# Optimization experiments

Hardware: AMD Instinct MI355X
Metric: run time of the kernel (lower is better)

Reference implementation:

```python
import jax, jax.numpy as jnp
import numpy as np
from jax import lax

ALPHA = 2.0
T_TAGS = 8  # number of distinct connects tags
ANCHOR_POS_FACTOR = jnp.array([1.0, 1.0], dtype=jnp.float32)
POS_FACTOR = [2.0, 1.0]  # [4,4,4,2,1][-2:]
NEG_FACTOR = [2.0, 1.0]


def setup_inputs() -> dict:
    key = jax.random.key(0)
    ks = jax.random.split(key, 10)
    B, A, M = 2, 2, 64
    Da, Db = 128, 64
    logits_a = jax.random.normal(ks[0], (B, A, Da, Da, Da), dtype=jnp.float32)
    logits_b = jax.random.normal(ks[1], (B, A, Db, Db, Db), dtype=jnp.float32)
    # GT prob maps: background labeled -1 (negmask), sparse positives labeled 1
    prob_a = jnp.where(jax.random.uniform(ks[2], (B, A, Da, Da, Da)) < 0.995, -1.0, 1.0).astype(jnp.float32)
    prob_b = jnp.where(jax.random.uniform(ks[3], (B, A, Db, Db, Db)) < 0.995, -1.0, 1.0).astype(jnp.float32)
    connects_a = jax.random.randint(ks[4], (B, A, Da, Da, Da), 0, T_TAGS, dtype=jnp.int32)
    connects_b = jax.random.randint(ks[5], (B, A, Db, Db, Db), 0, T_TAGS, dtype=jnp.int32)
    def make_coord(k, D):
        ka, kz = jax.random.split(k)
        anc = jax.random.randint(ka, (B, M, 1), 0, A, dtype=jnp.int32)
        sp = jax.random.randint(kz, (B, M, 3), 0, D, dtype=jnp.int32)
        c = jnp.concatenate([anc, sp], axis=-1)
        # pad last quarter of rows with -1 (invalid), as in the original padded coord lists
        c = c.at[:, 3 * M // 4:, :].set(-1)
        return c
    coord_a = make_coord(ks[6], Da)
    coord_b = make_coord(ks[7], Db)
    fnames = jnp.arange(B, dtype=jnp.float32)
    return {"logits_a": logits_a, "logits_b": logits_b, "prob_a": prob_a, "prob_b": prob_b,
            "connects_a": connects_a, "connects_b": connects_b,
            "coord_a": coord_a, "coord_b": coord_b, "fnames": fnames}


def _level_loss(logits, prob_gt, connects, coord, pos_f, neg_f):
    # ---- negative branch: sigmoid/logsigmoid elementwise + NMS maxpool mask ----
    prob = jax.nn.sigmoid(logits)
    nll = -jax.nn.log_sigmoid(-logits)  # -log(1 - sigmoid(logit))
    negmask = (prob_gt == -1.0).astype(logits.dtype)
    # max_pool3d kernel 3, stride 1, pad 1 over (D,H,W); anchors are channels
    pooled = lax.reduce_window(prob, -jnp.inf, lax.max,
                               (1, 1, 3, 3, 3), (1, 1, 1, 1, 1), 'SAME')
    max_filter = lax.stop_gradient((pooled == prob).astype(logits.dtype))
    negmask = negmask * max_filter
    w_neg = lax.stop_gradient(prob) ** ALPHA * negmask
    loss_neg = jnp.sum(nll * w_neg) * neg_f
    count_neg = jnp.sum(w_neg)
    wsum_neg = jnp.sum(w_neg) * neg_f

    # ---- positive branch: batched gather at coords (pad rows = -1) ----
    B, M, _ = coord.shape
    valid = coord[:, :, 0] > -1                       # [B, M]
    c = jnp.where(valid[..., None], coord, 0)         # safe indices
    b_idx = jnp.arange(B)[:, None]
    lp = logits[b_idx, c[..., 0], c[..., 1], c[..., 2], c[..., 3]]  # [B, M]
    pp = jax.nn.sigmoid(lp)
    w1 = (1.0 - lax.stop_gradient(pp)) ** ALPHA
    w2 = ANCHOR_POS_FACTOR[c[..., 0]]
    vf = valid.astype(logits.dtype)
    loss_pos = -jnp.sum(jax.nn.log_sigmoid(lp) * w1 * w2 * vf) * pos_f
    count_pos = jnp.sum(w1 * vf)
    wsum_pos = jnp.sum(w1 * w2 * vf) * pos_f

    # ---- connects-tag segment-min grouping (torch.unique + per-tag min) ----
    tags = connects[b_idx, c[..., 0], c[..., 1], c[..., 2], c[..., 3]]  # [B, M]
    seg = (jnp.arange(B, dtype=jnp.int32)[:, None] * T_TAGS + tags).reshape(-1)
    data = jnp.where(valid, w1, jnp.inf).reshape(-1)
    seg_min = jax.ops.segment_min(data, seg, num_segments=B * T_TAGS).reshape(B, T_TAGS)
    seg_min = jnp.where(jnp.isfinite(seg_min), seg_min, -1.0)  # absent tags -> -1 sentinel
    return loss_pos, loss_neg, count_pos, count_neg, wsum_pos, wsum_neg, seg_min


def reference(logits_a, logits_b, prob_a, prob_b, connects_a, connects_b, coord_a, coord_b, fnames):
    ra = _level_loss(logits_a, prob_a, connects_a, coord_a, POS_FACTOR[0], NEG_FACTOR[0])
    rb = _level_loss(logits_b, prob_b, connects_b, coord_b, POS_FACTOR[1], NEG_FACTOR[1])
    cls_loss_pos = ra[0] + rb[0]
    cls_loss_neg = ra[1] + rb[1]
    count_pos = ra[2] + rb[2]
    count_neg = ra[3] + rb[3]
    wsum_pos = ra[4] + rb[4]
    wsum_neg = ra[5] + rb[5]
    # pred_prob summary: per (level, sample, tag) min positive weight; fnames broadcast alongside
    pred_prob_min = jnp.stack([ra[6], rb[6]], axis=0)  # [2, B, T_TAGS]
    return (cls_loss_pos, cls_loss_neg, count_pos, count_neg, wsum_pos, wsum_neg, pred_prob_min)
```

## Files before the change

kernel.cpp:

```cpp
#include <hip/hip_runtime.h>
#include <math.h>


#define NBLK_A 1024
#define NBLK_B 256
#define NBLK_TOTAL (NBLK_A + NBLK_B + 1)

__device__ __forceinline__ float fmax3(float a, float b, float c) {
    return fmaxf(a, fmaxf(b, c));
}

__global__ __launch_bounds__(256, 3) void fused_kernel(
    const float* __restrict__ la, const float* __restrict__ lb,
    const float* __restrict__ ga, const float* __restrict__ gb,
    const int* __restrict__ conn_a, const int* __restrict__ conn_b,
    const int* __restrict__ coord_a, const int* __restrict__ coord_b,
    float* __restrict__ ws, float* __restrict__ out)
{
    __shared__ float tile[12800];
    __shared__ float sred[8];
    const int bid = blockIdx.x;
    const int t = threadIdx.x;
    float loss = 0.0f, wsum = 0.0f;
    int accIdx = -1;

    if (bid < NBLK_A) {
        accIdx = 0;
        const int vol = bid >> 8;
        const int ti = bid & 255;
        const int y0 = (ti & 15) << 3;
        const int z0 = (ti >> 4) << 3;
        const float* base = la + vol * (128 * 128 * 128);

        float4 stg[13];
        int us[13];
#pragma unroll
        for (int i = 0; i < 13; ++i) {
            int u = t + 256 * i; u = u < 3199 ? u : 3199;
            us[i] = u;
            int r = u >> 5, xq = u & 31;
            int rz = r / 10, ry = r - rz * 10;
            int gy = y0 - 1 + ry; gy = gy < 0 ? 0 : (gy > 127 ? 127 : gy);
            int gz = z0 - 1 + rz; gz = gz < 0 ? 0 : (gz > 127 ? 127 : gz);
            stg[i] = *(const float4*)(base + (gz * 128 + gy) * 128 + (xq << 2));
        }
#pragma unroll
        for (int i = 0; i < 13; ++i)
            *(float4*)(tile + (us[i] << 2)) = stg[i];
        __syncthreads();

        const int xq = t & 31, w = t >> 5;
        const int x0 = xq << 2;
        const int y = y0 + w;
        const float* gbase = ga + ((vol * 128 + z0) * 128 + y) * 128 + x0;
        float4 g[8];
#pragma unroll
        for (int zi = 0; zi < 8; ++zi) g[zi] = *(const float4*)(gbase + zi * 16384);

        float pm[3][4];
        float cm[2][4];
#pragma unroll
        for (int p = 0; p < 10; ++p) {
            const float* r0 = tile + (p * 10 + w) * 128 + x0;
            float4 a0 = *(const float4*)(r0);
            float4 a1 = *(const float4*)(r0 + 128);
            float4 a2 = *(const float4*)(r0 + 256);
            pm[p % 3][0] = fmax3(a0.x, a1.x, a2.x);
            pm[p % 3][1] = fmax3(a0.y, a1.y, a2.y);
            pm[p % 3][2] = fmax3(a0.z, a1.z, a2.z);
            pm[p % 3][3] = fmax3(a0.w, a1.w, a2.w);
            cm[p & 1][0] = a1.x; cm[p & 1][1] = a1.y;
            cm[p & 1][2] = a1.z; cm[p & 1][3] = a1.w;
            if (p >= 2) {
                float cz0 = fmax3(pm[0][0], pm[1][0], pm[2][0]);
                float cz1 = fmax3(pm[0][1], pm[1][1], pm[2][1]);
                float cz2 = fmax3(pm[0][2], pm[1][2], pm[2][2]);
                float cz3 = fmax3(pm[0][3], pm[1][3], pm[2][3]);
                float lco = __shfl_up(cz3, 1);  if (xq == 0)  lco = cz0;
                float rco = __shfl_down(cz0, 1); if (xq == 31) rco = cz3;
                float m0 = fmax3(lco, cz0, cz1);
                float m1 = fmax3(cz0, cz1, cz2);
                float m2 = fmax3(cz1, cz2, cz3);
                float m3 = fmax3(cz2, cz3, rco);
                const float* c = cm[(p - 1) & 1];
                float4 gv = g[p - 2];
                float ms[4] = {m0, m1, m2, m3};
                float gs[4] = {gv.x, gv.y, gv.z, gv.w};
#pragma unroll
                for (int k = 0; k < 4; ++k) {
                    if (gs[k] == -1.0f && ms[k] == c[k]) {
                        float e = __expf(c[k]);
                        float u = __builtin_amdgcn_rcpf(1.0f + e);
                        float sc = e * u;
                        float wv = sc * sc;
                        wsum += wv;
                        loss += (-__logf(u)) * wv;
                    }
                }
            }
        }
    } else if (bid < NBLK_A + NBLK_B) {
        accIdx = 2;
        const int b2 = bid - NBLK_A;
        const int vol = b2 >> 6;
        const int ti = b2 & 63;
        const int y0 = (ti & 7) << 3;
        const int z0 = (ti >> 3) << 3;
        const float* base = lb + vol * (64 * 64 * 64);

        float4 stg[7];
        int us[7];
#pragma unroll
        for (int i = 0; i < 7; ++i) {
            int u = t + 256 * i; u = u < 1599 ? u : 1599;
            us[i] = u;
            int r = u >> 4, xq = u & 15;
            int rz = r / 10, ry = r - rz * 10;
            int gy = y0 - 1 + ry; gy = gy < 0 ? 0 : (gy > 63 ? 63 : gy);
            int gz = z0 - 1 + rz; gz = gz < 0 ? 0 : (gz > 63 ? 63 : gz);
            stg[i] = *(const float4*)(base + (gz * 64 + gy) * 64 + (xq << 2));
        }
#pragma unroll
        for (int i = 0; i < 7; ++i)
            *(float4*)(tile + (us[i] << 2)) = stg[i];
        __syncthreads();

        const int xq = t & 15, grp = t >> 4;
        const int x0 = xq << 2;
        const int wy = grp & 7, zh = grp >> 3;
        const int y = y0 + wy;
        const float* gbase = gb + ((vol * 64 + z0 + 4 * zh) * 64 + y) * 64 + x0;
        float4 g[4];
#pragma unroll
        for (int j = 0; j < 4; ++j) g[j] = *(const float4*)(gbase + j * 4096);

        float pm[3][4];
        float cm[2][4];
#pragma unroll
        for (int pp = 0; pp < 6; ++pp) {
            const int rz = 4 * zh + pp;
            const float* r0 = tile + (rz * 10 + wy) * 64 + x0;
            float4 a0 = *(const float4*)(r0);
            float4 a1 = *(const float4*)(r0 + 64);
            float4 a2 = *(const float4*)(r0 + 128);
            pm[pp % 3][0] = fmax3(a0.x, a1.x, a2.x);
            pm[pp % 3][1] = fmax3(a0.y, a1.y, a2.y);
            pm[pp % 3][2] = fmax3(a0.z, a1.z, a2.z);
            pm[pp % 3][3] = fmax3(a0.w, a1.w, a2.w);
            cm[pp & 1][0] = a1.x; cm[pp & 1][1] = a1.y;
            cm[pp & 1][2] = a1.z; cm[pp & 1][3] = a1.w;
            if (pp >= 2) {
                float cz0 = fmax3(pm[0][0], pm[1][0], pm[2][0]);
                float cz1 = fmax3(pm[0][1], pm[1][1], pm[2][1]);
                float cz2 = fmax3(pm[0][2], pm[1][2], pm[2][2]);
                float cz3 = fmax3(pm[0][3], pm[1][3], pm[2][3]);
                float lco = __shfl_up(cz3, 1);  if (xq == 0)  lco = cz0;
                float rco = __shfl_down(cz0, 1); if (xq == 15) rco = cz3;
                float m0 = fmax3(lco, cz0, cz1);
                float m1 = fmax3(cz0, cz1, cz2);
                float m2 = fmax3(cz1, cz2, cz3);
                float m3 = fmax3(cz2, cz3, rco);
                const float* c = cm[(pp - 1) & 1];
                float4 gv = g[pp - 2];
                float ms[4] = {m0, m1, m2, m3};
                float gs[4] = {gv.x, gv.y, gv.z, gv.w};
#pragma unroll
                for (int k = 0; k < 4; ++k) {
                    if (gs[k] == -1.0f && ms[k] == c[k]) {
                        float e = __expf(c[k]);
                        float u = __builtin_amdgcn_rcpf(1.0f + e);
                        float sc = e * u;
                        float wv = sc * sc;
                        wsum += wv;
                        loss += (-__logf(u)) * wv;
                    }
                }
            }
        }
    } else {
        float* w1s = tile;
        float* tgf = tile + 128;
        for (int level = 0; level < 2; ++level) {
            const float* logits = level ? lb : la;
            const int* conn = level ? conn_b : conn_a;
            const int* coord = level ? coord_b : coord_a;
            const int D = level ? 64 : 128;
            float li = 0.0f, ci = 0.0f;
            if (t < 128) {
                const int* c4 = coord + t * 4;
                int a = c4[0], zz = c4[1], yy = c4[2], xx = c4[3];
                bool valid = a > -1;
                int aa = valid ? a : 0, z2 = valid ? zz : 0,
                    y2 = valid ? yy : 0, x2 = valid ? xx : 0;
                int b = t >> 6;
                int off = (((b * 2 + aa) * D + z2) * D + y2) * D + x2;
                float lp = logits[off];
                int tag = conn[off];
                float s = 1.0f / (1.0f + expf(lp));
                float w1 = s * s;
                float vf = valid ? 1.0f : 0.0f;
                float sp = fmaxf(-lp, 0.0f) + log1pf(expf(-fabsf(lp)));
                li = sp * w1 * vf;
                ci = w1 * vf;
                w1s[t] = w1;
                tgf[t] = (float)(valid ? tag : -1);
            }
            for (int o = 32; o; o >>= 1) {
                li += __shfl_down(li, o);
                ci += __shfl_down(ci, o);
            }
            if ((t & 63) == 0) { sred[t >> 6] = li; sred[4 + (t >> 6)] = ci; }
            __syncthreads();
            if (t == 0) {
                atomicAdd(ws + 4 + 2 * level, sred[0] + sred[1] + sred[2] + sred[3]);
                atomicAdd(ws + 5 + 2 * level, sred[4] + sred[5] + sred[6] + sred[7]);
            }
            if (t < 16) {
                int bb = t >> 3, tg = t & 7;
                float mn = INFINITY;
                for (int i = 0; i < 64; ++i) {
                    int j = bb * 64 + i;
                    if (tgf[j] == (float)tg) mn = fminf(mn, w1s[j]);
                }
                out[6 + level * 16 + bb * 8 + tg] = isinf(mn) ? -1.0f : mn;
            }
            __syncthreads();
        }
    }

    if (accIdx >= 0) {
        for (int o = 32; o; o >>= 1) {
            loss += __shfl_down(loss, o);
            wsum += __shfl_down(wsum, o);
        }
        if ((t & 63) == 0) { sred[t >> 6] = loss; sred[4 + (t >> 6)] = wsum; }
        __syncthreads();
        if (t == 0) {
            float L = sred[0] + sred[1] + sred[2] + sred[3];
            float W = sred[4] + sred[5] + sred[6] + sred[7];
            if (L != 0.0f || W != 0.0f) {
                atomicAdd(ws + accIdx, L);
                atomicAdd(ws + accIdx + 1, W);
            }
        }
    }

    if (t == 0) {
        __threadfence();
        unsigned int old = atomicAdd((unsigned int*)(ws + 8), 1u);
        if (old == NBLK_TOTAL - 1) {
            float s0 = atomicAdd(ws + 0, 0.0f);
            float s1 = atomicAdd(ws + 1, 0.0f);
            float s2 = atomicAdd(ws + 2, 0.0f);
            float s3 = atomicAdd(ws + 3, 0.0f);
            float s4 = atomicAdd(ws + 4, 0.0f);
            float s5 = atomicAdd(ws + 5, 0.0f);
            float s6 = atomicAdd(ws + 6, 0.0f);
            float s7 = atomicAdd(ws + 7, 0.0f);
            out[0] = s4 * 2.0f + s6;
            out[1] = s0 * 2.0f + s2;
            out[2] = s5 + s7;
            out[3] = s1 + s3;
            out[4] = s5 * 2.0f + s7;
            out[5] = s1 * 2.0f + s3;
        }
    }
}

extern "C" void kernel_launch(void* const* d_in, const int* in_sizes, int n_in,
                              void* d_out, int out_size, void* d_ws, size_t ws_size,
                              hipStream_t stream) {
    const float* logits_a = (const float*)d_in[0];
    const float* logits_b = (const float*)d_in[1];
    const float* prob_a   = (const float*)d_in[2];
    const float* prob_b   = (const float*)d_in[3];
    const int*   conn_a   = (const int*)d_in[4];
    const int*   conn_b   = (const int*)d_in[5];
    const int*   coord_a  = (const int*)d_in[6];
    const int*   coord_b  = (const int*)d_in[7];
    float* out = (float*)d_out;
    float* ws  = (float*)d_ws;

    hipMemsetAsync(ws, 0, 12 * sizeof(float), stream);
    fused_kernel<<<NBLK_TOTAL, 256, 0, stream>>>(
        logits_a, logits_b, prob_a, prob_b,
        conn_a, conn_b, coord_a, coord_b, ws, out);
}
```

Baseline: 188.2 us.

## Replace LDS halo tiling with per-thread z-slice y-marching from global memory

Drops the 50KB shared-memory halo tile and its cooperative staging and barrier. Each thread now owns one z slice and marches along y, reading the three neighbouring z rows straight from global memory and relying on L1/L2 for halo reuse. Level-B block count is halved so each block covers 16 z slices, and launch bounds rise to 4 waves per SIMD because LDS no longer limits occupancy. In exchange, global and cache traffic rises, since each logit row is fetched by several threads instead of once per block.

```diff
diff --git a/kernel.cpp b/kernel.cpp
--- a/kernel.cpp
+++ b/kernel.cpp
@@ -3,22 +3,86 @@
 
 
 #define NBLK_A 1024
-#define NBLK_B 256
+#define NBLK_B 128
 #define NBLK_TOTAL (NBLK_A + NBLK_B + 1)
 
 __device__ __forceinline__ float fmax3(float a, float b, float c) {
     return fmaxf(a, fmaxf(b, c));
 }
 
-__global__ __launch_bounds__(256, 3) void fused_kernel(
+template <int D, int LOG2D, int XQ>
+__device__ __forceinline__ void neg_march(
+    const float* __restrict__ logits, const float* __restrict__ gt,
+    int vol, int z, int y0, int xq, float& loss, float& wsum)
+{
+    const int x0 = xq << 2;
+    const float* vb = logits + (vol << (3 * LOG2D));
+    const int zm = z > 0 ? z - 1 : 0;
+    const int zp = z < D - 1 ? z + 1 : z;
+    const float* pzm = vb + (zm << (2 * LOG2D));
+    const float* pz0 = vb + (z << (2 * LOG2D));
+    const float* pzp = vb + (zp << (2 * LOG2D));
+    const float* pg = gt + (vol << (3 * LOG2D)) + (z << (2 * LOG2D));
+
+    float zw[3][4];
+    float cc[2][4];
+    float4 gg[2];
+
+#pragma unroll
+    for (int s = 0; s < 10; ++s) {
+        int yy = y0 - 1 + s;
+        yy = yy < 0 ? 0 : (yy > D - 1 ? D - 1 : yy);
+        const int ro = (yy << LOG2D) + x0;
+        float4 r0 = *(const float4*)(pzm + ro);
+        float4 r1 = *(const float4*)(pz0 + ro);
+        float4 r2 = *(const float4*)(pzp + ro);
+        if (s >= 1 && s <= 8) gg[s & 1] = *(const float4*)(pg + ro);
+        zw[s % 3][0] = fmax3(r0.x, r1.x, r2.x);
+        zw[s % 3][1] = fmax3(r0.y, r1.y, r2.y);
+        zw[s % 3][2] = fmax3(r0.z, r1.z, r2.z);
+        zw[s % 3][3] = fmax3(r0.w, r1.w, r2.w);
+        cc[s & 1][0] = r1.x; cc[s & 1][1] = r1.y;
+        cc[s & 1][2] = r1.z; cc[s & 1][3] = r1.w;
+        if (s >= 2) {
+            float cz0 = fmax3(zw[0][0], zw[1][0], zw[2][0]);
+            float cz1 = fmax3(zw[0][1], zw[1][1], zw[2][1]);
+            float cz2 = fmax3(zw[0][2], zw[1][2], zw[2][2]);
+            float cz3 = fmax3(zw[0][3], zw[1][3], zw[2][3]);
+            float lco = __shfl_up(cz3, 1);   if (xq == 0)      lco = cz0;
+            float rco = __shfl_down(cz0, 1); if (xq == XQ - 1) rco = cz3;
+            float m0 = fmax3(lco, cz0, cz1);
+            float m1 = fmax3(cz0, cz1, cz2);
+            float m2 = fmax3(cz1, cz2, cz3);
+            float m3 = fmax3(cz2, cz3, rco);
+            const float* c = cc[(s - 1) & 1];
+            float4 gq = gg[(s - 1) & 1];
+            float ms[4] = {m0, m1, m2, m3};
+            float gs[4] = {gq.x, gq.y, gq.z, gq.w};
+#pragma unroll
+            for (int k = 0; k < 4; ++k) {
+                if (gs[k] == -1.0f && ms[k] == c[k]) {
+                    float e = __expf(c[k]);
+                    float u = __builtin_amdgcn_rcpf(1.0f + e);
+                    float sc = e * u;
+                    float wv = sc * sc;
+                    wsum += wv;
+                    loss += (-__logf(u)) * wv;
+                }
+            }
+        }
+    }
+}
+
+__global__ __launch_bounds__(256, 4) void fused_kernel(
     const float* __restrict__ la, const float* __restrict__ lb,
     const float* __restrict__ ga, const float* __restrict__ gb,
     const int* __restrict__ conn_a, const int* __restrict__ conn_b,
     const int* __restrict__ coord_a, const int* __restrict__ coord_b,
     float* __restrict__ ws, float* __restrict__ out)
 {
-    __shared__ float tile[12800];
     __shared__ float sred[8];
+    __shared__ float w1s[128];
+    __shared__ float tgf[128];
     const int bid = blockIdx.x;
     const int t = threadIdx.x;
     float loss = 0.0f, wsum = 0.0f;
@@ -27,159 +91,19 @@
     if (bid < NBLK_A) {
         accIdx = 0;
         const int vol = bid >> 8;
-        const int ti = bid & 255;
-        const int y0 = (ti & 15) << 3;
-        const int z0 = (ti >> 4) << 3;
-        const float* base = la + vol * (128 * 128 * 128);
-
-        float4 stg[13];
-        int us[13];
-#pragma unroll
-        for (int i = 0; i < 13; ++i) {
-            int u = t + 256 * i; u = u < 3199 ? u : 3199;
-            us[i] = u;
-            int r = u >> 5, xq = u & 31;
-            int rz = r / 10, ry = r - rz * 10;
-            int gy = y0 - 1 + ry; gy = gy < 0 ? 0 : (gy > 127 ? 127 : gy);
-            int gz = z0 - 1 + rz; gz = gz < 0 ? 0 : (gz > 127 ? 127 : gz);
-            stg[i] = *(const float4*)(base + (gz * 128 + gy) * 128 + (xq << 2));
-        }
-#pragma unroll
-        for (int i = 0; i < 13; ++i)
-            *(float4*)(tile + (us[i] << 2)) = stg[i];
-        __syncthreads();
-
-        const int xq = t & 31, w = t >> 5;
-        const int x0 = xq << 2;
-        const int y = y0 + w;
-        const float* gbase = ga + ((vol * 128 + z0) * 128 + y) * 128 + x0;
-        float4 g[8];
-#pragma unroll
-        for (int zi = 0; zi < 8; ++zi) g[zi] = *(const float4*)(gbase + zi * 16384);
-
-        float pm[3][4];
-        float cm[2][4];
-#pragma unroll
-        for (int p = 0; p < 10; ++p) {
-            const float* r0 = tile + (p * 10 + w) * 128 + x0;
-            float4 a0 = *(const float4*)(r0);
-            float4 a1 = *(const float4*)(r0 + 128);
-            float4 a2 = *(const float4*)(r0 + 256);
-            pm[p % 3][0] = fmax3(a0.x, a1.x, a2.x);
-            pm[p % 3][1] = fmax3(a0.y, a1.y, a2.y);
-            pm[p % 3][2] = fmax3(a0.z, a1.z, a2.z);
-            pm[p % 3][3] = fmax3(a0.w, a1.w, a2.w);
-            cm[p & 1][0] = a1.x; cm[p & 1][1] = a1.y;
-            cm[p & 1][2] = a1.z; cm[p & 1][3] = a1.w;
-            if (p >= 2) {
-                float cz0 = fmax3(pm[0][0], pm[1][0], pm[2][0]);
-                float cz1 = fmax3(pm[0][1], pm[1][1], pm[2][1]);
-                float cz2 = fmax3(pm[0][2], pm[1][2], pm[2][2]);
-                float cz3 = fmax3(pm[0][3], pm[1][3], pm[2][3]);
-                float lco = __shfl_up(cz3, 1);  if (xq == 0)  lco = cz0;
-                float rco = __shfl_down(cz0, 1); if (xq == 31) rco = cz3;
-                float m0 = fmax3(lco, cz0, cz1);
-                float m1 = fmax3(cz0, cz1, cz2);
-                float m2 = fmax3(cz1, cz2, cz3);
-                float m3 = fmax3(cz2, cz3, rco);
-                const float* c = cm[(p - 1) & 1];
-                float4 gv = g[p - 2];
-                float ms[4] = {m0, m1, m2, m3};
-                float gs[4] = {gv.x, gv.y, gv.z, gv.w};
-#pragma unroll
-                for (int k = 0; k < 4; ++k) {
-                    if (gs[k] == -1.0f && ms[k] == c[k]) {
-                        float e = __expf(c[k]);
-                        float u = __builtin_amdgcn_rcpf(1.0f + e);
-                        float sc = e * u;
-                        float wv = sc * sc;
-                        wsum += wv;
-                        loss += (-__logf(u)) * wv;
-                    }
-                }
-            }
-        }
+        const int rem = bid & 255;
+        const int zb = rem >> 4, yc = rem & 15;
+        neg_march<128, 7, 32>(la, ga, vol, zb * 8 + (t >> 5), yc * 8, t & 31,
+                              loss, wsum);
     } else if (bid < NBLK_A + NBLK_B) {
         accIdx = 2;
         const int b2 = bid - NBLK_A;
-        const int vol = b2 >> 6;
-        const int ti = b2 & 63;
-        const int y0 = (ti & 7) << 3;
-        const int z0 = (ti >> 3) << 3;
-        const float* base = lb + vol * (64 * 64 * 64);
-
-        float4 stg[7];
-        int us[7];
-#pragma unroll
-        for (int i = 0; i < 7; ++i) {
-            int u = t + 256 * i; u = u < 1599 ? u : 1599;
-            us[i] = u;
-            int r = u >> 4, xq = u & 15;
-            int rz = r / 10, ry = r - rz * 10;
-            int gy = y0 - 1 + ry; gy = gy < 0 ? 0 : (gy > 63 ? 63 : gy);
-            int gz = z0 - 1 + rz; gz = gz < 0 ? 0 : (gz > 63 ? 63 : gz);
-            stg[i] = *(const float4*)(base + (gz * 64 + gy) * 64 + (xq << 2));
-        }
-#pragma unroll
-        for (int i = 0; i < 7; ++i)
-            *(float4*)(tile + (us[i] << 2)) = stg[i];
-        __syncthreads();
-
-        const int xq = t & 15, grp = t >> 4;
-        const int x0 = xq << 2;
-        const int wy = grp & 7, zh = grp >> 3;
-        const int y = y0 + wy;
-        const float* gbase = gb + ((vol * 64 + z0 + 4 * zh) * 64 + y) * 64 + x0;
-        float4 g[4];
-#pragma unroll
-        for (int j = 0; j < 4; ++j) g[j] = *(const float4*)(gbase + j * 4096);
-
-        float pm[3][4];
-        float cm[2][4];
-#pragma unroll
-        for (int pp = 0; pp < 6; ++pp) {
-            const int rz = 4 * zh + pp;
-            const float* r0 = tile + (rz * 10 + wy) * 64 + x0;
-            float4 a0 = *(const float4*)(r0);
-            float4 a1 = *(const float4*)(r0 + 64);
-            float4 a2 = *(const float4*)(r0 + 128);
-            pm[pp % 3][0] = fmax3(a0.x, a1.x, a2.x);
-            pm[pp % 3][1] = fmax3(a0.y, a1.y, a2.y);
-            pm[pp % 3][2] = fmax3(a0.z, a1.z, a2.z);
-            pm[pp % 3][3] = fmax3(a0.w, a1.w, a2.w);
-            cm[pp & 1][0] = a1.x; cm[pp & 1][1] = a1.y;
-            cm[pp & 1][2] = a1.z; cm[pp & 1][3] = a1.w;
-            if (pp >= 2) {
-                float cz0 = fmax3(pm[0][0], pm[1][0], pm[2][0]);
-                float cz1 = fmax3(pm[0][1], pm[1][1], pm[2][1]);
-                float cz2 = fmax3(pm[0][2], pm[1][2], pm[2][2]);
-                float cz3 = fmax3(pm[0][3], pm[1][3], pm[2][3]);
-                float lco = __shfl_up(cz3, 1);  if (xq == 0)  lco = cz0;
-                float rco = __shfl_down(cz0, 1); if (xq == 15) rco = cz3;
-                float m0 = fmax3(lco, cz0, cz1);
-                float m1 = fmax3(cz0, cz1, cz2);
-                float m2 = fmax3(cz1, cz2, cz3);
-                float m3 = fmax3(cz2, cz3, rco);
-                const float* c = cm[(pp - 1) & 1];
-                float4 gv = g[pp - 2];
-                float ms[4] = {m0, m1, m2, m3};
-                float gs[4] = {gv.x, gv.y, gv.z, gv.w};
-#pragma unroll
-                for (int k = 0; k < 4; ++k) {
-                    if (gs[k] == -1.0f && ms[k] == c[k]) {
-                        float e = __expf(c[k]);
-                        float u = __builtin_amdgcn_rcpf(1.0f + e);
-                        float sc = e * u;
-                        float wv = sc * sc;
-                        wsum += wv;
-                        loss += (-__logf(u)) * wv;
-                    }
-                }
-            }
-        }
+        const int vol = b2 >> 5;
+        const int rem = b2 & 31;
+        const int zb = rem >> 3, yc = rem & 7;
+        neg_march<64, 6, 16>(lb, gb, vol, zb * 16 + (t >> 4), yc * 8, t & 15,
+                             loss, wsum);
     } else {
-        float* w1s = tile;
-        float* tgf = tile + 128;
         for (int level = 0; level < 2; ++level) {
             const float* logits = level ? lb : la;
             const int* conn = level ? conn_b : conn_a;
```

Result: faster. 178.5 us (-5.1%).
